# Optimization experiments

Measured on AMD Instinct MI355X. Metric: run time of the kernel, lower is better.

The kernel has to match this reference:

```python
import jax, jax.numpy as jnp
import numpy as np

R = 2          # total_rel
N = 6144       # total_ent / num nodes
H1 = 256       # layer 1 out
H2 = 256       # layer 2 out


def setup_inputs() -> dict:
    key = jax.random.key(0)
    k_adj, k_w1, k_c1, k_w2, k_c2 = jax.random.split(key, 5)
    adj = jax.random.uniform(k_adj, (R, N, N), dtype=jnp.float32)
    bw1 = jax.random.normal(k_w1, (R, N, H1), dtype=jnp.float32) * (1.0 / np.sqrt(N))
    bc1 = jax.random.normal(k_c1, (R, R), dtype=jnp.float32)
    bw2 = jax.random.normal(k_w2, (R, H1, H2), dtype=jnp.float32) * (1.0 / np.sqrt(H1))
    bc2 = jax.random.normal(k_c2, (R, R), dtype=jnp.float32)
    return {"adj": adj, "bw1": bw1, "bc1": bc1, "bw2": bw2, "bc2": bc2}


def _layer_weights(coeff, basis):
    # (R, n_basis) x (n_basis, in, out) -> (R*in, out)
    w = jnp.einsum('ij,jmn->imn', coeff, basis)
    return w.reshape(w.shape[0] * w.shape[1], w.shape[2])


def reference(adj, bw1, bc1, bw2, bc2):
    # --- layer 1: node_init is None -> features are dense adjacencies ---
    w1 = _layer_weights(bc1, bw1)                        # (R*N, H1)
    # cat([adj[0], adj[1]], axis=1) == transpose+reshape  (N, R*N)
    tmp1 = adj.transpose(1, 0, 2).reshape(N, R * N)
    out1 = tmp1 @ w1                                     # (N, H1)

    # --- layer 2: relu then per-relation spmm + basis matmul ---
    x = jax.nn.relu(out1)
    w2 = _layer_weights(bc2, bw2)                        # (R*H1, H2)
    # cat([adj[r] @ x for r], axis=1) as one einsum       (N, R*H1)
    tmp2 = jnp.einsum('rij,jd->ird', adj, x).reshape(N, R * H1)
    out2 = tmp2 @ w2                                     # (N, H2)

    final_rep = jnp.concatenate([out1, out2], axis=1)    # (N, H1+H2)
    final_rep = jnp.sum(final_rep, axis=0).reshape(-1, H1 + H2)  # (1, H1+H2)
    return (out2, final_rep)
```

## Files before the change

kernel.cpp:

```cpp
#include <hip/hip_runtime.h>


#define NN 6144
#define HH 256
#define SPLIT 8
#define KCHUNK 1536
#define KSTEPS 24

typedef __attribute__((ext_vector_type(4))) float f32x4;
typedef __attribute__((ext_vector_type(8))) unsigned short u16x8;
typedef __attribute__((ext_vector_type(4))) unsigned short u16x4;

__device__ __forceinline__ unsigned short f2bf(float f) {
  unsigned int u = __float_as_uint(f);
  u += 0x7FFFu + ((u >> 16) & 1u);
  return (unsigned short)(u >> 16);
}

__device__ __forceinline__ void mfma_bf16(f32x4& d, u16x8 a, u16x8 b) {
  asm("v_mfma_f32_16x16x32_bf16 %0, %1, %2, %0" : "+v"(d) : "v"(a), "v"(b));
}

__global__ void wgen_kernel(const float* __restrict__ basis,
                            const float* __restrict__ bc,
                            unsigned short* __restrict__ outw,
                            int tilesPerR, int jdim)
{
  __shared__ unsigned short wt[64][265];
  const int t  = blockIdx.x;
  const int r  = t / tilesPerR;
  const int jt = t % tilesPerR;
  const float c0 = bc[r * 2 + 0];
  const float c1 = bc[r * 2 + 1];
  const int tid = threadIdx.x;
  const float* b0 = basis + (size_t)jt * 64 * HH;
  const float* b1 = basis + (size_t)jdim * HH + (size_t)jt * 64 * HH;
#pragma unroll
  for (int k = 0; k < 16; ++k) {
    int idx = tid + k * 256;
    int row = idx >> 6;
    int c4  = (idx & 63) * 4;
    f32x4 v0 = *(const f32x4*)(b0 + (size_t)row * HH + c4);
    f32x4 v1 = *(const f32x4*)(b1 + (size_t)row * HH + c4);
    wt[row][c4 + 0] = f2bf(c0 * v0.x + c1 * v1.x);
    wt[row][c4 + 1] = f2bf(c0 * v0.y + c1 * v1.y);
    wt[row][c4 + 2] = f2bf(c0 * v0.z + c1 * v1.z);
    wt[row][c4 + 3] = f2bf(c0 * v0.w + c1 * v1.w);
  }
  __syncthreads();
#pragma unroll
  for (int k = 0; k < 8; ++k) {
    int chunk = tid + k * 256;
    int h  = chunk >> 3;
    int sp = chunk & 7;
    int j0 = (sp ^ (h & 7)) * 8;
    u16x8 v;
#pragma unroll
    for (int e = 0; e < 8; ++e) v[e] = wt[j0 + e][h];
    *(u16x8*)(outw + ((size_t)t * 2048 + chunk) * 8) = v;
  }
}

__global__ __launch_bounds__(256, 2) void gemm_adj_kernel(
    const float* __restrict__ adj, const unsigned short* __restrict__ Bws,
    float* __restrict__ Pp)
{
  __shared__ __align__(16) unsigned short Alds[64 * 64];
  __shared__ __align__(16) unsigned short Blds[256 * 64];
  const int tid  = threadIdx.x;
  const int lane = tid & 63;
  const int wave = tid >> 6;
  const int mb = blockIdx.x;
  const int s  = blockIdx.y;
  const int i0 = mb * 64;
  const int kbase = s * KCHUNK;
  const int rrel  = kbase / NN;
  const int jb    = kbase % NN;
  const int tBase = kbase / 64;

  const float* aRow = adj + (size_t)rrel * NN * NN
                      + (size_t)(i0 + (tid >> 4)) * NN + jb + (tid & 15) * 4;
  const unsigned short* bBase = Bws + (size_t)tBase * 2048 * 8 + (size_t)tid * 8;

  f32x4 acc[4][4];
#pragma unroll
  for (int m = 0; m < 4; ++m)
#pragma unroll
    for (int n = 0; n < 4; ++n) acc[m][n] = (f32x4){0.f, 0.f, 0.f, 0.f};

  for (int kk = 0; kk < KSTEPS; ++kk) {
    f32x4 av[4];
#pragma unroll
    for (int it = 0; it < 4; ++it)
      av[it] = *(const f32x4*)(aRow + (size_t)it * 16 * NN + kk * 64);
    u16x8 bv[8];
#pragma unroll
    for (int c = 0; c < 8; ++c)
      bv[c] = *(const u16x8*)(bBase + (size_t)kk * 2048 * 8 + c * 256 * 8);
    __syncthreads();
#pragma unroll
    for (int it = 0; it < 4; ++it) {
      int row = (tid >> 4) + it * 16;
      int off = ((tid & 15) * 8) ^ ((row & 7) << 4);
      u16x4 w;
      w[0] = f2bf(av[it].x); w[1] = f2bf(av[it].y);
      w[2] = f2bf(av[it].z); w[3] = f2bf(av[it].w);
      *(u16x4*)((char*)Alds + row * 128 + off) = w;
    }
#pragma unroll
    for (int c = 0; c < 8; ++c)
      *(u16x8*)(Blds + ((size_t)c * 256 + tid) * 8) = bv[c];
    __syncthreads();
#pragma unroll
    for (int ks = 0; ks < 2; ++ks) {
      u16x8 af[4], bfr[4];
#pragma unroll
      for (int m = 0; m < 4; ++m) {
        int row = m * 16 + (lane & 15);
        int off = (ks * 64 + ((lane >> 4) << 4)) ^ ((row & 7) << 4);
        af[m] = *(const u16x8*)((const char*)Alds + row * 128 + off);
      }
#pragma unroll
      for (int n = 0; n < 4; ++n) {
        int row = wave * 64 + n * 16 + (lane & 15);
        int off = (ks * 64 + ((lane >> 4) << 4)) ^ ((row & 7) << 4);
        bfr[n] = *(const u16x8*)((const char*)Blds + row * 128 + off);
      }
#pragma unroll
      for (int m = 0; m < 4; ++m)
#pragma unroll
        for (int n = 0; n < 4; ++n)
          mfma_bf16(acc[m][n], af[m], bfr[n]);
    }
  }
  float* P = Pp + ((size_t)s * NN + i0) * HH;
#pragma unroll
  for (int m = 0; m < 4; ++m)
#pragma unroll
    for (int n = 0; n < 4; ++n) {
      int col = wave * 64 + n * 16 + (lane & 15);
#pragma unroll
      for (int q = 0; q < 4; ++q) {
        int row = m * 16 + ((lane >> 4) << 2) + q;
        P[(size_t)row * HH + col] = acc[m][n][q];
      }
    }
}

__global__ __launch_bounds__(256, 2) void gemm_y_kernel(
    const unsigned short* __restrict__ xws, const unsigned short* __restrict__ w2ws,
    unsigned short* __restrict__ B2ws)
{
  __shared__ __align__(16) unsigned short Alds[64 * 64];
  __shared__ __align__(16) unsigned short Blds[256 * 64];
  const int tid  = threadIdx.x;
  const int lane = tid & 63;
  const int wave = tid >> 6;
  const int mb = blockIdx.x;
  const int r  = blockIdx.y;

  f32x4 acc[4][4];
#pragma unroll
  for (int m = 0; m < 4; ++m)
#pragma unroll
    for (int n = 0; n < 4; ++n) acc[m][n] = (f32x4){0.f, 0.f, 0.f, 0.f};

  for (int dt = 0; dt < 4; ++dt) {
    u16x8 avv[2];
    avv[0] = *(const u16x8*)(xws + (((size_t)(mb * 4 + dt)) * 512 + tid) * 8);
    avv[1] = *(const u16x8*)(xws + (((size_t)(mb * 4 + dt)) * 512 + 256 + tid) * 8);
    u16x8 bv[8];
#pragma unroll
    for (int c = 0; c < 8; ++c)
      bv[c] = *(const u16x8*)(w2ws + (((size_t)(r * 4 + dt)) * 2048 + c * 256 + tid) * 8);
    __syncthreads();
    *(u16x8*)(Alds + (size_t)tid * 8) = avv[0];
    *(u16x8*)(Alds + ((size_t)256 + tid) * 8) = avv[1];
#pragma unroll
    for (int c = 0; c < 8; ++c)
      *(u16x8*)(Blds + ((size_t)c * 256 + tid) * 8) = bv[c];
    __syncthreads();
#pragma unroll
    for (int ks = 0; ks < 2; ++ks) {
      u16x8 af[4], bfr[4];
#pragma unroll
      for (int m = 0; m < 4; ++m) {
        int row = m * 16 + (lane & 15);
        int off = (ks * 64 + ((lane >> 4) << 4)) ^ ((row & 7) << 4);
        af[m] = *(const u16x8*)((const char*)Alds + row * 128 + off);
      }
#pragma unroll
      for (int n = 0; n < 4; ++n) {
        int row = wave * 64 + n * 16 + (lane & 15);
        int off = (ks * 64 + ((lane >> 4) << 4)) ^ ((row & 7) << 4);
        bfr[n] = *(const u16x8*)((const char*)Blds + row * 128 + off);
      }
#pragma unroll
      for (int m = 0; m < 4; ++m)
#pragma unroll
        for (int n = 0; n < 4; ++n)
          mfma_bf16(acc[m][n], af[m], bfr[n]);
    }
  }
  const int tg = r * 96 + mb;
#pragma unroll
  for (int m = 0; m < 4; ++m) {
    int scont = m * 2 + ((lane >> 4) >> 1);
    int e0    = ((lane >> 4) & 1) * 4;
#pragma unroll
    for (int n = 0; n < 4; ++n) {
      int h   = wave * 64 + n * 16 + (lane & 15);
      int pos = scont ^ (h & 7);
      u16x4 v;
      v[0] = f2bf(acc[m][n][0]); v[1] = f2bf(acc[m][n][1]);
      v[2] = f2bf(acc[m][n][2]); v[3] = f2bf(acc[m][n][3]);
      *(u16x4*)(B2ws + (((size_t)tg * 2048 + h * 8 + pos) * 8 + e0)) = v;
    }
  }
}

__global__ void reduce1_kernel(const float* __restrict__ Pp, float* __restrict__ out1,
                               unsigned short* __restrict__ xws)
{
  const int tid = threadIdx.x;
  const int b   = blockIdx.x;
  const int hc  = tid & 31;
  const int rg  = tid >> 5;
  const int dt    = hc >> 3;
  const int scont = hc & 7;
  for (int k = 0; k < 8; ++k) {
    int i = b * 64 + rg + k * 8;
    f32x4 s0 = (f32x4){0.f, 0.f, 0.f, 0.f};
    f32x4 s1 = (f32x4){0.f, 0.f, 0.f, 0.f};
#pragma unroll
    for (int s = 0; s < SPLIT; ++s) {
      const float* p = Pp + ((size_t)s * NN + i) * HH + hc * 8;
      s0 += *(const f32x4*)p;
      s1 += *(const f32x4*)(p + 4);
    }
    float* o = out1 + (size_t)i * HH + hc * 8;
    *(f32x4*)o = s0;
    *(f32x4*)(o + 4) = s1;
    u16x8 xv;
    xv[0] = f2bf(fmaxf(s0.x, 0.f)); xv[1] = f2bf(fmaxf(s0.y, 0.f));
    xv[2] = f2bf(fmaxf(s0.z, 0.f)); xv[3] = f2bf(fmaxf(s0.w, 0.f));
    xv[4] = f2bf(fmaxf(s1.x, 0.f)); xv[5] = f2bf(fmaxf(s1.y, 0.f));
    xv[6] = f2bf(fmaxf(s1.z, 0.f)); xv[7] = f2bf(fmaxf(s1.w, 0.f));
    int pos = scont ^ (i & 7);
    *(u16x8*)(xws + (((size_t)(b * 4 + dt)) * 512 + (i & 63) * 8 + pos) * 8) = xv;
  }
}

__global__ void reduce2_kernel(const float* __restrict__ Pp, float* __restrict__ outp)
{
  const int tid = threadIdx.x;
  const int b   = blockIdx.x;
  const int hc  = tid & 31;
  const int rg  = tid >> 5;
  for (int k = 0; k < 8; ++k) {
    int i = b * 64 + rg + k * 8;
    f32x4 s0 = (f32x4){0.f, 0.f, 0.f, 0.f};
    f32x4 s1 = (f32x4){0.f, 0.f, 0.f, 0.f};
#pragma unroll
    for (int s = 0; s < SPLIT; ++s) {
      const float* p = Pp + ((size_t)s * NN + i) * HH + hc * 8;
      s0 += *(const f32x4*)p;
      s1 += *(const f32x4*)(p + 4);
    }
    float* o = outp + (size_t)i * HH + hc * 8;
    *(f32x4*)o = s0;
    *(f32x4*)(o + 4) = s1;
  }
}

__global__ void zero_fin_kernel(float* fin) {
  fin[blockIdx.x * 256 + threadIdx.x] = 0.f;
}

__global__ void colsum_kernel(const float* __restrict__ out1,
                              const float* __restrict__ out2,
                              float* __restrict__ fin)
{
  const int t = threadIdx.x;
  const float* src = blockIdx.y ? out2 : out1;
  size_t i0 = (size_t)blockIdx.x * 64;
  float s = 0.f;
  for (int rr = 0; rr < 64; ++rr) s += src[(i0 + rr) * HH + t];
  atomicAdd(&fin[blockIdx.y * HH + t], s);
}

extern "C" void kernel_launch(void* const* d_in, const int* in_sizes, int n_in,
                              void* d_out, int out_size, void* d_ws, size_t ws_size,
                              hipStream_t stream)
{
  const float* adj = (const float*)d_in[0];
  const float* bw1 = (const float*)d_in[1];
  const float* bc1 = (const float*)d_in[2];
  const float* bw2 = (const float*)d_in[3];
  const float* bc2 = (const float*)d_in[4];
  float* out2 = (float*)d_out;
  float* fin  = (float*)d_out + (size_t)NN * HH;

  char* ws = (char*)d_ws;
  float*          Pp   = (float*)(ws + 0);
  unsigned short* B1ws = (unsigned short*)(ws + 50331648);
  unsigned short* B2ws = (unsigned short*)(ws + 56623104);
  float*          out1 = (float*)(ws + 62914560);
  unsigned short* xws  = (unsigned short*)(ws + 69206016);
  unsigned short* w2ws = (unsigned short*)(ws + 72351744);

  zero_fin_kernel<<<2, 256, 0, stream>>>(fin);
  wgen_kernel<<<192, 256, 0, stream>>>(bw1, bc1, B1ws, 96, NN);
  gemm_adj_kernel<<<dim3(96, SPLIT), 256, 0, stream>>>(adj, B1ws, Pp);
  reduce1_kernel<<<96, 256, 0, stream>>>(Pp, out1, xws);
  wgen_kernel<<<8, 256, 0, stream>>>(bw2, bc2, w2ws, 4, HH);
  gemm_y_kernel<<<dim3(96, 2), 256, 0, stream>>>(xws, w2ws, B2ws);
  gemm_adj_kernel<<<dim3(96, SPLIT), 256, 0, stream>>>(adj, B2ws, Pp);
  reduce2_kernel<<<96, 256, 0, stream>>>(Pp, out2);
  colsum_kernel<<<dim3(96, 2), 256, 0, stream>>>(out1, out2, fin);
}
```

Before: 232.3 us.

## Prefetch next K tile, store split-K partials as bf16, fuse colsum into reductions

The adjacency GEMM now issues the global loads for step k+1 right after the LDS barrier, so they overlap the MFMAs of step k. Launch bounds rise to 3 blocks per SM to raise occupancy. Split-K partials are written as bf16 instead of fp32, halving partial-buffer traffic. The column sums are folded into the reduce kernels, which removes the out1 buffer and the separate colsum pass. Rounding partials to bf16 before summation adds precision loss, and the larger live register set from prefetching may conflict with the tighter launch bound.

```diff
diff --git a/kernel.cpp b/kernel.cpp
--- a/kernel.cpp
+++ b/kernel.cpp
@@ -15,6 +15,9 @@
   unsigned int u = __float_as_uint(f);
   u += 0x7FFFu + ((u >> 16) & 1u);
   return (unsigned short)(u >> 16);
+}
+__device__ __forceinline__ float bf2f(unsigned short h) {
+  return __uint_as_float(((unsigned int)h) << 16);
 }
 
 __device__ __forceinline__ void mfma_bf16(f32x4& d, u16x8 a, u16x8 b) {
@@ -61,9 +64,9 @@
   }
 }
 
-__global__ __launch_bounds__(256, 2) void gemm_adj_kernel(
+__global__ __launch_bounds__(256, 3) void gemm_adj_kernel(
     const float* __restrict__ adj, const unsigned short* __restrict__ Bws,
-    float* __restrict__ Pp)
+    unsigned short* __restrict__ Pp)
 {
   __shared__ __align__(16) unsigned short Alds[64 * 64];
   __shared__ __align__(16) unsigned short Blds[256 * 64];
@@ -88,15 +91,21 @@
 #pragma unroll
     for (int n = 0; n < 4; ++n) acc[m][n] = (f32x4){0.f, 0.f, 0.f, 0.f};
 
+  f32x4 av[4];
+  u16x8 bv[8];
+
+#define LOADK(KK) do {                                                        \
+    _Pragma("unroll")                                                         \
+    for (int it = 0; it < 4; ++it)                                            \
+      av[it] = *(const f32x4*)(aRow + (size_t)it * 16 * NN + (KK) * 64);      \
+    _Pragma("unroll")                                                         \
+    for (int c = 0; c < 8; ++c)                                               \
+      bv[c] = *(const u16x8*)(bBase + (size_t)(KK) * 2048 * 8 + c * 256 * 8); \
+  } while (0)
+
+  LOADK(0);
+
   for (int kk = 0; kk < KSTEPS; ++kk) {
-    f32x4 av[4];
-#pragma unroll
-    for (int it = 0; it < 4; ++it)
-      av[it] = *(const f32x4*)(aRow + (size_t)it * 16 * NN + kk * 64);
-    u16x8 bv[8];
-#pragma unroll
-    for (int c = 0; c < 8; ++c)
-      bv[c] = *(const u16x8*)(bBase + (size_t)kk * 2048 * 8 + c * 256 * 8);
     __syncthreads();
 #pragma unroll
     for (int it = 0; it < 4; ++it) {
@@ -111,6 +120,7 @@
     for (int c = 0; c < 8; ++c)
       *(u16x8*)(Blds + ((size_t)c * 256 + tid) * 8) = bv[c];
     __syncthreads();
+    if (kk + 1 < KSTEPS) LOADK(kk + 1);
 #pragma unroll
     for (int ks = 0; ks < 2; ++ks) {
       u16x8 af[4], bfr[4];
@@ -133,7 +143,8 @@
           mfma_bf16(acc[m][n], af[m], bfr[n]);
     }
   }
-  float* P = Pp + ((size_t)s * NN + i0) * HH;
+#undef LOADK
+  unsigned short* P = Pp + ((size_t)s * NN + i0) * HH;
 #pragma unroll
   for (int m = 0; m < 4; ++m)
 #pragma unroll
@@ -142,7 +153,7 @@
 #pragma unroll
       for (int q = 0; q < 4; ++q) {
         int row = m * 16 + ((lane >> 4) << 2) + q;
-        P[(size_t)row * HH + col] = acc[m][n][q];
+        P[(size_t)row * HH + col] = f2bf(acc[m][n][q]);
       }
     }
 }
@@ -219,74 +230,81 @@
   }
 }
 
-__global__ void reduce1_kernel(const float* __restrict__ Pp, float* __restrict__ out1,
-                               unsigned short* __restrict__ xws)
-{
+__global__ void reduce1_kernel(const unsigned short* __restrict__ Pp,
+                               unsigned short* __restrict__ xws,
+                               float* __restrict__ fin)
+{
+  __shared__ float csm[8][256];
   const int tid = threadIdx.x;
   const int b   = blockIdx.x;
   const int hc  = tid & 31;
   const int rg  = tid >> 5;
   const int dt    = hc >> 3;
   const int scont = hc & 7;
+  float cs[8] = {0.f, 0.f, 0.f, 0.f, 0.f, 0.f, 0.f, 0.f};
   for (int k = 0; k < 8; ++k) {
     int i = b * 64 + rg + k * 8;
-    f32x4 s0 = (f32x4){0.f, 0.f, 0.f, 0.f};
-    f32x4 s1 = (f32x4){0.f, 0.f, 0.f, 0.f};
+    float sv[8] = {0.f, 0.f, 0.f, 0.f, 0.f, 0.f, 0.f, 0.f};
 #pragma unroll
     for (int s = 0; s < SPLIT; ++s) {
-      const float* p = Pp + ((size_t)s * NN + i) * HH + hc * 8;
-      s0 += *(const f32x4*)p;
-      s1 += *(const f32x4*)(p + 4);
-    }
-    float* o = out1 + (size_t)i * HH + hc * 8;
-    *(f32x4*)o = s0;
-    *(f32x4*)(o + 4) = s1;
+      u16x8 v = *(const u16x8*)(Pp + ((size_t)s * NN + i) * HH + hc * 8);
+#pragma unroll
+      for (int e = 0; e < 8; ++e) sv[e] += bf2f(v[e]);
+    }
     u16x8 xv;
-    xv[0] = f2bf(fmaxf(s0.x, 0.f)); xv[1] = f2bf(fmaxf(s0.y, 0.f));
-    xv[2] = f2bf(fmaxf(s0.z, 0.f)); xv[3] = f2bf(fmaxf(s0.w, 0.f));
-    xv[4] = f2bf(fmaxf(s1.x, 0.f)); xv[5] = f2bf(fmaxf(s1.y, 0.f));
-    xv[6] = f2bf(fmaxf(s1.z, 0.f)); xv[7] = f2bf(fmaxf(s1.w, 0.f));
+#pragma unroll
+    for (int e = 0; e < 8; ++e) {
+      cs[e] += sv[e];
+      xv[e] = f2bf(fmaxf(sv[e], 0.f));
+    }
     int pos = scont ^ (i & 7);
     *(u16x8*)(xws + (((size_t)(b * 4 + dt)) * 512 + (i & 63) * 8 + pos) * 8) = xv;
   }
-}
-
-__global__ void reduce2_kernel(const float* __restrict__ Pp, float* __restrict__ outp)
-{
+#pragma unroll
+  for (int e = 0; e < 8; ++e) csm[rg][hc * 8 + e] = cs[e];
+  __syncthreads();
+  float v = 0.f;
+#pragma unroll
+  for (int r8 = 0; r8 < 8; ++r8) v += csm[r8][tid];
+  atomicAdd(&fin[tid], v);
+}
+
+__global__ void reduce2_kernel(const unsigned short* __restrict__ Pp,
+                               float* __restrict__ outp,
+                               float* __restrict__ fin)
+{
+  __shared__ float csm[8][256];
   const int tid = threadIdx.x;
   const int b   = blockIdx.x;
   const int hc  = tid & 31;
   const int rg  = tid >> 5;
+  float cs[8] = {0.f, 0.f, 0.f, 0.f, 0.f, 0.f, 0.f, 0.f};
   for (int k = 0; k < 8; ++k) {
     int i = b * 64 + rg + k * 8;
-    f32x4 s0 = (f32x4){0.f, 0.f, 0.f, 0.f};
-    f32x4 s1 = (f32x4){0.f, 0.f, 0.f, 0.f};
+    float sv[8] = {0.f, 0.f, 0.f, 0.f, 0.f, 0.f, 0.f, 0.f};
 #pragma unroll
     for (int s = 0; s < SPLIT; ++s) {
-      const float* p = Pp + ((size_t)s * NN + i) * HH + hc * 8;
-      s0 += *(const f32x4*)p;
-      s1 += *(const f32x4*)(p + 4);
+      u16x8 v = *(const u16x8*)(Pp + ((size_t)s * NN + i) * HH + hc * 8);
+#pragma unroll
+      for (int e = 0; e < 8; ++e) sv[e] += bf2f(v[e]);
     }
     float* o = outp + (size_t)i * HH + hc * 8;
-    *(f32x4*)o = s0;
-    *(f32x4*)(o + 4) = s1;
-  }
+    *(f32x4*)o = (f32x4){sv[0], sv[1], sv[2], sv[3]};
+    *(f32x4*)(o + 4) = (f32x4){sv[4], sv[5], sv[6], sv[7]};
+#pragma unroll
+    for (int e = 0; e < 8; ++e) cs[e] += sv[e];
+  }
+#pragma unroll
+  for (int e = 0; e < 8; ++e) csm[rg][hc * 8 + e] = cs[e];
+  __syncthreads();
+  float v = 0.f;
+#pragma unroll
+  for (int r8 = 0; r8 < 8; ++r8) v += csm[r8][tid];
+  atomicAdd(&fin[256 + tid], v);
 }
 
 __global__ void zero_fin_kernel(float* fin) {
   fin[blockIdx.x * 256 + threadIdx.x] = 0.f;
-}
-
-__global__ void colsum_kernel(const float* __restrict__ out1,
-                              const float* __restrict__ out2,
-                              float* __restrict__ fin)
-{
-  const int t = threadIdx.x;
-  const float* src = blockIdx.y ? out2 : out1;
-  size_t i0 = (size_t)blockIdx.x * 64;
-  float s = 0.f;
-  for (int rr = 0; rr < 64; ++rr) s += src[(i0 + rr) * HH + t];
-  atomicAdd(&fin[blockIdx.y * HH + t], s);
 }
 
 extern "C" void kernel_launch(void* const* d_in, const int* in_sizes, int n_in,
@@ -302,20 +320,18 @@
   float* fin  = (float*)d_out + (size_t)NN * HH;
 
   char* ws = (char*)d_ws;
-  float*          Pp   = (float*)(ws + 0);
-  unsigned short* B1ws = (unsigned short*)(ws + 50331648);
-  unsigned short* B2ws = (unsigned short*)(ws + 56623104);
-  float*          out1 = (float*)(ws + 62914560);
-  unsigned short* xws  = (unsigned short*)(ws + 69206016);
-  unsigned short* w2ws = (unsigned short*)(ws + 72351744);
+  unsigned short* Pp   = (unsigned short*)(ws + 0);
+  unsigned short* B1ws = (unsigned short*)(ws + 25165824);
+  unsigned short* B2ws = (unsigned short*)(ws + 31457280);
+  unsigned short* xws  = (unsigned short*)(ws + 37748736);
+  unsigned short* w2ws = (unsigned short*)(ws + 40894464);
 
   zero_fin_kernel<<<2, 256, 0, stream>>>(fin);
   wgen_kernel<<<192, 256, 0, stream>>>(bw1, bc1, B1ws, 96, NN);
   gemm_adj_kernel<<<dim3(96, SPLIT), 256, 0, stream>>>(adj, B1ws, Pp);
-  reduce1_kernel<<<96, 256, 0, stream>>>(Pp, out1, xws);
+  reduce1_kernel<<<96, 256, 0, stream>>>(Pp, xws, fin);
   wgen_kernel<<<8, 256, 0, stream>>>(bw2, bc2, w2ws, 4, HH);
   gemm_y_kernel<<<dim3(96, 2), 256, 0, stream>>>(xws, w2ws, B2ws);
   gemm_adj_kernel<<<dim3(96, SPLIT), 256, 0, stream>>>(adj, B2ws, Pp);
-  reduce2_kernel<<<96, 256, 0, stream>>>(Pp, out2);
-  colsum_kernel<<<dim3(96, 2), 256, 0, stream>>>(out1, out2, fin);
-}
+  reduce2_kernel<<<96, 256, 0, stream>>>(Pp, out2, fin);
+}
```

Result: faster. 203.7 us (-12.3%).
